# Optimization experiments

Hardware: AMD Instinct MI355X
Metric: run time of the kernel (lower is better)

Reference implementation:

```python
import math
import jax, jax.numpy as jnp
import numpy as np

B, T, C = 1, 2048, 2048
H, G, D = 16, 4, 128          # n_head, n_query_groups, head_size; C == H*D
Q_PER_KV = H // G
EPS = 1e-5


def _apply_rope_interleaved(x, cos, sin):
    # x: [B, T, h, D]; cos/sin: [T, D//2]; interleaved (GPT-J) style pairs
    x1 = x[..., 0::2]
    x2 = x[..., 1::2]
    c = cos[None, :, None, :]
    s = sin[None, :, None, :]
    o1 = x1 * c - x2 * s
    o2 = x1 * s + x2 * c
    return jnp.stack([o1, o2], axis=-1).reshape(x.shape)


def setup_inputs() -> dict:
    key = jax.random.key(0)
    k0, k1, k2, k3 = jax.random.split(key, 4)
    x = jax.random.normal(k0, (B, T, C), jnp.float32)
    # rotary cache (standard theta=10000)
    inv_freq = 1.0 / (10000.0 ** (np.arange(0, D, 2, dtype=np.float64) / D))
    ang = np.outer(np.arange(T, dtype=np.float64), inv_freq)
    cos = jnp.asarray(np.cos(ang), jnp.float32)
    sin = jnp.asarray(np.sin(ang), jnp.float32)
    # RetNet per-head decay mask: D[h,i,j] = gamma_h^(i-j) for i>=j else 0
    gammas = 1.0 - 2.0 ** (-5.0 - np.arange(H, dtype=np.float64))
    i = np.arange(T)[:, None]
    j = np.arange(T)[None, :]
    diff = np.maximum(i - j, 0).astype(np.float64)
    m = np.where(i >= j, gammas[:, None, None] ** diff[None], 0.0)
    mask = jnp.asarray(m, jnp.float32)
    std = 0.02
    W_reten = jax.random.normal(k1, (C, (H + 2 * G) * D), jnp.float32) * std
    W_gate = jax.random.normal(k2, (C, C), jnp.float32) * std
    W_proj = jax.random.normal(k3, (C, C), jnp.float32) * std
    return {"x": x, "cos": cos, "sin": sin, "mask": mask,
            "W_reten": W_reten, "W_gate": W_gate, "W_proj": W_proj,
            "max_seq_length": T}


def reference(x, cos, sin, mask, W_reten, W_gate, W_proj, max_seq_length):
    # fused qkv projection, grouped-query layout
    qkv = (x @ W_reten).reshape(B, T, G, Q_PER_KV + 2, D)
    q = qkv[..., :Q_PER_KV, :].reshape(B, T, H, D)
    k = qkv[..., Q_PER_KV:Q_PER_KV + 1, :].reshape(B, T, G, D)
    v = qkv[..., Q_PER_KV + 1:, :].reshape(B, T, G, D)
    q = _apply_rope_interleaved(q, cos, sin)
    k = _apply_rope_interleaved(k, cos, sin)
    # [B, h, T, D]
    q = q.transpose(0, 2, 1, 3)
    k = jnp.repeat(k.transpose(0, 2, 1, 3), Q_PER_KV, axis=1)
    v = jnp.repeat(v.transpose(0, 2, 1, 3), Q_PER_KV, axis=1)
    # parallel retention: masked (decay) scores, no softmax
    scale = 1.0 / math.sqrt(D)
    qk = jnp.einsum('bhtd,bhsd->bhts', q, k) * scale
    qk = qk * mask[None]
    y = jnp.einsum('bhts,bhsd->bhtd', qk, v)
    # group norm = RMSNorm (no weight) over head_size
    y = y.transpose(0, 2, 1, 3)  # [B, T, H, D]
    y = y * jax.lax.rsqrt(jnp.mean(y * y, axis=-1, keepdims=True) + EPS)
    y = y.reshape(B, T, C)
    g = jax.nn.silu(x @ W_gate)
    return (g * y) @ W_proj
```

## Files before the change

### kernel.cpp

```cpp
#include <hip/hip_runtime.h>
#include <hip/hip_bf16.h>
#include <cstdint>
#include <cstddef>

typedef __bf16 bf16x8 __attribute__((ext_vector_type(8)));
typedef __bf16 bf16x4 __attribute__((ext_vector_type(4)));
typedef __bf16 bf16x2 __attribute__((ext_vector_type(2)));
typedef float  f32x4  __attribute__((ext_vector_type(4)));
typedef float  f32x2  __attribute__((ext_vector_type(2)));

#define T_SEQ 2048
#define CDIM  2048
#define NH    16
#define NG    4
#define DH    128
#define NCHUNK 32

__device__ __forceinline__ void gl_lds16(const __bf16* g, __bf16* l) {
  __builtin_amdgcn_global_load_lds(
      (const __attribute__((address_space(1))) void*)g,
      (__attribute__((address_space(3))) void*)l, 16, 0, 0);
}

__global__ __launch_bounds__(256) void pre_kernel(
    const float* __restrict__ x, const float* __restrict__ Wr,
    const float* __restrict__ Wg, const float* __restrict__ Wp,
    __bf16* __restrict__ xb, __bf16* __restrict__ wtb, __bf16* __restrict__ wpb) {
  __shared__ __bf16 tile[64][68];
  int bid = blockIdx.x;
  int tid = threadIdx.x;
  if (bid < 2048) {
    size_t i = ((size_t)bid * 256 + tid) * 8;
    f32x4 a = *(const f32x4*)(x + i);
    f32x4 b = *(const f32x4*)(x + i + 4);
    bf16x8 o;
#pragma unroll
    for (int j = 0; j < 4; ++j) { o[j] = (__bf16)a[j]; o[4 + j] = (__bf16)b[j]; }
    *(bf16x8*)(xb + i) = o;
    return;
  }
  int rel = bid - 2048;
  const float* W; __bf16* Wt; int N;
  if (rel < 1536)      { W = Wr; Wt = wtb;                        N = 3072; }
  else if (rel < 2560) { W = Wg; Wt = wtb + (size_t)3072 * CDIM;  N = 2048; rel -= 1536; }
  else                 { W = Wp; Wt = wpb;                        N = 2048; rel -= 2560; }
  const int K = 2048;
  int k0 = (rel & 31) * 64, n0 = (rel >> 5) * 64;
  int c4 = (tid & 15) * 4, r = tid >> 4;
#pragma unroll
  for (int rr = 0; rr < 4; ++rr) {
    int row = r + rr * 16;
    f32x4 v = *(const f32x4*)(W + (size_t)(k0 + row) * N + n0 + c4);
#pragma unroll
    for (int j = 0; j < 4; ++j) tile[row][c4 + j] = (__bf16)v[j];
  }
  __syncthreads();
  int n = tid >> 2, seg = tid & 3;
  __bf16 vals[16];
#pragma unroll
  for (int j = 0; j < 16; ++j) vals[j] = tile[seg * 16 + j][n];
  __bf16* dst = Wt + (size_t)(n0 + n) * K + k0 + seg * 16;
  *(bf16x8*)(dst)     = *(bf16x8*)(&vals[0]);
  *(bf16x8*)(dst + 8) = *(bf16x8*)(&vals[8]);
}

__global__ __launch_bounds__(256) void ropevt_kernel(const float* __restrict__ qkv,
    const float* __restrict__ cosb, const float* __restrict__ sinb,
    __bf16* __restrict__ qb, __bf16* __restrict__ kb, __bf16* __restrict__ vtb) {
  __shared__ __bf16 vt[64][136];
  int bid = blockIdx.x;
  int tid = threadIdx.x;
  if (bid < 2048) {
    int t = bid;
    int w = tid >> 6, l = tid & 63;
    float c = cosb[t * 64 + l], s = sinb[t * 64 + l];
#pragma unroll
    for (int it = 0; it < 5; ++it) {
      int slot = w + it * 4;
      int g = slot / 5, j = slot % 5;
      const float* src = qkv + (size_t)t * 3072 + g * 768 + j * 128;
      f32x2 xv = *(const f32x2*)(src + 2 * l);
      bf16x2 o;
      o[0] = (__bf16)(xv[0] * c - xv[1] * s);
      o[1] = (__bf16)(xv[0] * s + xv[1] * c);
      __bf16* dst = (j < 4) ? (qb + ((size_t)(g * 4 + j) * T_SEQ + t) * DH)
                            : (kb + ((size_t)g * T_SEQ + t) * DH);
      *(bf16x2*)(dst + 2 * l) = o;
    }
    return;
  }
  int rel = bid - 2048;
  int g = rel >> 5, t0 = (rel & 31) * 64;
#pragma unroll
  for (int it = 0; it < 8; ++it) {
    int q = it * 256 + tid;
    int tt = q >> 5, dq = q & 31;
    f32x4 v = *(const f32x4*)(qkv + (size_t)(t0 + tt) * 3072 + g * 768 + 640 + dq * 4);
#pragma unroll
    for (int j = 0; j < 4; ++j) vt[tt][dq * 4 + j] = (__bf16)v[j];
  }
  __syncthreads();
  int d = tid >> 1, half = tid & 1;
  __bf16 outv[32];
#pragma unroll
  for (int j = 0; j < 32; ++j) outv[j] = vt[half * 32 + j][d];
  __bf16* dst = vtb + ((size_t)g * DH + d) * T_SEQ + t0 + half * 32;
#pragma unroll
  for (int q4 = 0; q4 < 4; ++q4) *(bf16x8*)(dst + q4 * 8) = *(bf16x8*)(&outv[q4 * 8]);
}

__global__ __launch_bounds__(256) void kt_kernel(const __bf16* __restrict__ kb,
                                                 __bf16* __restrict__ ktb) {
  __shared__ __bf16 tile[64][136];
  int g = blockIdx.x >> 5, t0 = (blockIdx.x & 31) * 64;
  int tid = threadIdx.x;
#pragma unroll
  for (int it = 0; it < 4; ++it) {
    int fg = it * 256 + tid;
    int tt = fg >> 4, gr = fg & 15;
    bf16x8 v = *(const bf16x8*)(kb + ((size_t)g * T_SEQ + t0 + tt) * DH + gr * 8);
    *(bf16x8*)(&tile[tt][gr * 8]) = v;
  }
  __syncthreads();
  int d = tid >> 1, half = tid & 1;
  __bf16 outv[32];
#pragma unroll
  for (int j = 0; j < 32; ++j) outv[j] = tile[half * 32 + j][d];
  __bf16* dst = ktb + ((size_t)g * DH + d) * T_SEQ + t0 + half * 32;
#pragma unroll
  for (int q4 = 0; q4 < 4; ++q4) *(bf16x8*)(dst + q4 * 8) = *(bf16x8*)(&outv[q4 * 8]);
}

__global__ __launch_bounds__(256) void u_kernel(const __bf16* __restrict__ vtb,
                                                const __bf16* __restrict__ ktb,
                                                float* __restrict__ Ut) {
  int h = blockIdx.x >> 5, c = blockIdx.x & 31, g = h >> 2;
  int tid = threadIdx.x;
  int w = tid >> 6, l = tid & 63, lr = l & 15, lg = l >> 4;
  float l2g = log2f(1.0f - exp2f(-5.0f - (float)h));
  float ginv = exp2f(-l2g);
  f32x4 acc[2][8] = {};
#pragma unroll
  for (int kk = 0; kk < 2; ++kk) {
    int j0 = kk * 32 + lg * 8;
    float w0 = exp2f(l2g * (float)(64 - j0));
    bf16x8 aw[2];
#pragma unroll
    for (int i = 0; i < 2; ++i) {
      bf16x8 av = *(const bf16x8*)(vtb + ((size_t)g * DH + w * 32 + i * 16 + lr) * T_SEQ
                                   + c * 64 + j0);
      float wj = w0;
#pragma unroll
      for (int jj = 0; jj < 8; ++jj) { aw[i][jj] = (__bf16)((float)av[jj] * wj); wj *= ginv; }
    }
#pragma unroll
    for (int jf = 0; jf < 8; ++jf) {
      bf16x8 bv = *(const bf16x8*)(ktb + ((size_t)g * DH + jf * 16 + lr) * T_SEQ
                                   + c * 64 + j0);
      acc[0][jf] = __builtin_amdgcn_mfma_f32_16x16x32_bf16(aw[0], bv, acc[0][jf], 0, 0, 0);
      acc[1][jf] = __builtin_amdgcn_mfma_f32_16x16x32_bf16(aw[1], bv, acc[1][jf], 0, 0, 0);
    }
  }
  float* outb = Ut + (size_t)blockIdx.x * 16384;
#pragma unroll
  for (int i = 0; i < 2; ++i)
#pragma unroll
    for (int jf = 0; jf < 8; ++jf)
#pragma unroll
      for (int r = 0; r < 4; ++r)
        outb[(w * 32 + i * 16 + lg * 4 + r) * 128 + jf * 16 + lr] = acc[i][jf][r];
}

__global__ __launch_bounds__(256) void scan_kernel(const float* __restrict__ Ut,
                                                   __bf16* __restrict__ St) {
  int bid = blockIdx.x, tid = threadIdx.x;
  int h = bid >> 4;
  int row = ((bid >> 1) & 7) * 16 + (tid >> 4);
  int col = (bid & 1) * 64 + (tid & 15) * 4;
  float l2g = log2f(1.0f - exp2f(-5.0f - (float)h));
  float df = exp2f(l2g * 64.0f);
  f32x4 s = {0.f, 0.f, 0.f, 0.f};
  for (int c = 0; c < NCHUNK; ++c) {
    size_t base = ((size_t)(h * NCHUNK + c) * 128 + row) * 128 + col;
    bf16x4 o;
#pragma unroll
    for (int j = 0; j < 4; ++j) o[j] = (__bf16)s[j];
    *(bf16x4*)(St + base) = o;
    f32x4 u = *(const f32x4*)(Ut + base);
#pragma unroll
    for (int j = 0; j < 4; ++j) s[j] = df * s[j] + u[j];
  }
}

__global__ __launch_bounds__(256) void attn2_kernel(const __bf16* __restrict__ qb,
    const __bf16* __restrict__ kb, const __bf16* __restrict__ vtb,
    const __bf16* __restrict__ St, float* __restrict__ y) {
  __shared__ __bf16 kl[64 * 128];
  __shared__ __bf16 vl[128 * 64];
  __shared__ __bf16 pl[4][16 * 64];
  int h = blockIdx.x >> 5, qt = blockIdx.x & 31;
  int g = h >> 2;
  int w = threadIdx.x >> 6, l = threadIdx.x & 63;
  int lr = l & 15, lg = l >> 4;
  int t0b = qt * 64;
  int t0 = t0b + w * 16;
  bf16x8 qf[4];
#pragma unroll
  for (int kbk = 0; kbk < 4; ++kbk)
    qf[kbk] = *(const bf16x8*)(qb + ((size_t)h * T_SEQ + t0 + lr) * DH + kbk * 32 + lg * 8);
  float gamma = 1.0f - exp2f(-5.0f - (float)h);
  float l2g = log2f(gamma);
  const float scale = 0.088388347648318447f;
  int s0 = t0b;
#pragma unroll
  for (int it = 0; it < 4; ++it) {
    int fg = it * 256 + threadIdx.x;
    {
      int ss = fg >> 4, gr = fg & 15;
      bf16x8 kv = *(const bf16x8*)(kb + ((size_t)g * T_SEQ + s0 + ss) * DH + gr * 8);
      *(bf16x8*)((char*)kl + ss * 256 + ((gr * 16) ^ ((ss & 7) << 4))) = kv;
    }
    {
      int d = fg >> 3, gv = fg & 7;
      bf16x8 vv = *(const bf16x8*)(vtb + ((size_t)g * DH + d) * T_SEQ + s0 + gv * 8);
      *(bf16x8*)((char*)vl + d * 128 + ((gv * 16) ^ ((d & 7) << 4))) = vv;
    }
  }
  float wfac = scale * exp2f(l2g * (float)(w * 16 + lr));
  bf16x8 qwf[4];
#pragma unroll
  for (int kbk = 0; kbk < 4; ++kbk)
#pragma unroll
    for (int e = 0; e < 8; ++e) qwf[kbk][e] = (__bf16)((float)qf[kbk][e] * wfac);
  f32x4 acc[8] = {};
  const __bf16* Sb = St + (size_t)(h * NCHUNK + qt) * 16384;
#pragma unroll
  for (int dc = 0; dc < 8; ++dc)
#pragma unroll
    for (int kc = 0; kc < 4; ++kc) {
      bf16x8 sf = *(const bf16x8*)(Sb + (dc * 16 + lr) * 128 + kc * 32 + lg * 8);
      acc[dc] = __builtin_amdgcn_mfma_f32_16x16x32_bf16(qwf[kc], sf, acc[dc], 0, 0, 0);
    }
  __syncthreads();
#pragma unroll
  for (int sc = 0; sc < 4; ++sc) {
    f32x4 p = {0.f, 0.f, 0.f, 0.f};
    int srow = sc * 16 + lr;
#pragma unroll
    for (int kbk = 0; kbk < 4; ++kbk) {
      bf16x8 kf = *(const bf16x8*)((char*)kl + srow * 256 +
                                   ((kbk * 64 + lg * 16) ^ ((srow & 7) << 4)));
      p = __builtin_amdgcn_mfma_f32_16x16x32_bf16(qf[kbk], kf, p, 0, 0, 0);
    }
#pragma unroll
    for (int r = 0; r < 4; ++r) {
      int tl = lg * 4 + r;
      int diff = (w * 16 + tl) - srow;
      float val = 0.0f;
      if (diff >= 0) val = p[r] * scale * exp2f((float)diff * l2g);
      *(__bf16*)((char*)(pl[w]) + tl * 128 +
                 (((sc * 16 + lr) * 2) ^ ((tl & 7) << 4))) = (__bf16)val;
    }
  }
  bf16x8 pa[2];
#pragma unroll
  for (int kc = 0; kc < 2; ++kc)
    pa[kc] = *(const bf16x8*)((char*)(pl[w]) + lr * 128 +
                              ((kc * 64 + lg * 16) ^ ((lr & 7) << 4)));
#pragma unroll
  for (int dc = 0; dc < 8; ++dc) {
#pragma unroll
    for (int kc = 0; kc < 2; ++kc) {
      int vrow = dc * 16 + lr;
      bf16x8 vf = *(const bf16x8*)((char*)vl + vrow * 128 +
                                   ((kc * 64 + lg * 16) ^ ((vrow & 7) << 4)));
      acc[dc] = __builtin_amdgcn_mfma_f32_16x16x32_bf16(pa[kc], vf, acc[dc], 0, 0, 0);
    }
  }
#pragma unroll
  for (int dc = 0; dc < 8; ++dc)
#pragma unroll
    for (int r = 0; r < 4; ++r)
      y[((size_t)h * T_SEQ + t0 + lg * 4 + r) * DH + dc * 16 + lr] = acc[dc][r];
}

template<int MODE>
__global__ __launch_bounds__(256) void gemm_gl_kernel(
    const __bf16* __restrict__ A, const __bf16* __restrict__ Bt,
    float* __restrict__ Cf, __bf16* __restrict__ Cg, int M, int N, int K) {
  __shared__ __bf16 Asb[64 * 64];
  __shared__ __bf16 Bsb[128 * 64];
  int m0 = blockIdx.x * 64, n0 = blockIdx.y * 128;
  int tid = threadIdx.x;
  int w = tid >> 6, l = tid & 63;
  int wr = w >> 1, wc = w & 1;
  int lr = l & 15, lg = l >> 4;
  int nk = K >> 6;
  const __bf16* Ab = A + (size_t)m0 * K;
  const __bf16* Bb = Bt + (size_t)n0 * K;
  f32x4 acc[2][4] = {};
  for (int kt = 0; kt < nk; ++kt) {
    int k0 = kt << 6;
#pragma unroll
    for (int c = 0; c < 2; ++c) {
      int ca = c * 256 + tid;
      int row = ca >> 3, kseg = ca & 7;
      gl_lds16(Ab + (size_t)row * K + k0 + ((kseg ^ (row & 7)) << 3), Asb + ca * 8);
    }
#pragma unroll
    for (int c = 0; c < 4; ++c) {
      int cb = c * 256 + tid;
      int row = cb >> 3, kseg = cb & 7;
      gl_lds16(Bb + (size_t)row * K + k0 + ((kseg ^ (row & 7)) << 3), Bsb + cb * 8);
    }
    __syncthreads();
    bf16x8 av[2][2], bv[4][2];
#pragma unroll
    for (int i = 0; i < 2; ++i)
#pragma unroll
      for (int kk = 0; kk < 2; ++kk) {
        int row = wr * 32 + i * 16 + lr;
        av[i][kk] = *(const bf16x8*)((const char*)Asb +
            ((row * 128 + kk * 64 + lg * 16) ^ ((lr & 7) << 4)));
      }
#pragma unroll
    for (int j = 0; j < 4; ++j)
#pragma unroll
      for (int kk = 0; kk < 2; ++kk) {
        int row = wc * 64 + j * 16 + lr;
        bv[j][kk] = *(const bf16x8*)((const char*)Bsb +
            ((row * 128 + kk * 64 + lg * 16) ^ ((lr & 7) << 4)));
      }
#pragma unroll
    for (int kk = 0; kk < 2; ++kk)
#pragma unroll
      for (int i = 0; i < 2; ++i)
#pragma unroll
        for (int j = 0; j < 4; ++j)
          acc[i][j] = __builtin_amdgcn_mfma_f32_16x16x32_bf16(av[i][kk], bv[j][kk],
                                                              acc[i][j], 0, 0, 0);
    __syncthreads();
  }
#pragma unroll
  for (int i = 0; i < 2; ++i) {
    int row = m0 + wr * 32 + i * 16 + lg * 4;
#pragma unroll
    for (int j = 0; j < 4; ++j) {
      int col = n0 + wc * 64 + j * 16 + lr;
#pragma unroll
      for (int r = 0; r < 4; ++r) {
        float z = acc[i][j][r];
        if (MODE == 0) {
          Cf[(size_t)(row + r) * N + col] = z;
        } else {
          if (n0 < 3072) {
            Cf[(size_t)(row + r) * 3072 + col] = z;
          } else {
            float sv = z / (1.0f + expf(-z));
            Cg[(size_t)(row + r) * 2048 + (col - 3072)] = (__bf16)sv;
          }
        }
      }
    }
  }
}

__global__ __launch_bounds__(256) void rms_gate_kernel(const float* __restrict__ y,
                                                       const __bf16* __restrict__ gateb,
                                                       __bf16* __restrict__ ynormb) {
  int f = blockIdx.x * 4 + (threadIdx.x >> 6);
  int l = threadIdx.x & 63;
  int h = f >> 11, t = f & 2047;
  const float* row = y + (size_t)f * DH;
  f32x2 v = *(const f32x2*)(row + 2 * l);
  float ss = v[0] * v[0] + v[1] * v[1];
#pragma unroll
  for (int o = 32; o > 0; o >>= 1) ss += __shfl_xor(ss, o, 64);
  float r = rsqrtf(ss * (1.0f / 128.0f) + 1e-5f);
  size_t base = (size_t)t * CDIM + h * DH + 2 * l;
  bf16x2 gv = *(const bf16x2*)(gateb + base);
  bf16x2 o;
  o[0] = (__bf16)(v[0] * r * (float)gv[0]);
  o[1] = (__bf16)(v[1] * r * (float)gv[1]);
  *(bf16x2*)(ynormb + base) = o;
}

extern "C" void kernel_launch(void* const* d_in, const int* in_sizes, int n_in,
                              void* d_out, int out_size, void* d_ws, size_t ws_size,
                              hipStream_t stream) {
  const float* x    = (const float*)d_in[0];
  const float* cosb = (const float*)d_in[1];
  const float* sinb = (const float*)d_in[2];
  const float* Wr   = (const float*)d_in[4];
  const float* Wg   = (const float*)d_in[5];
  const float* Wp   = (const float*)d_in[6];

  char* ws = (char*)d_ws;
  size_t off = 0;
  auto alloc = [&](size_t bytes) { void* p = ws + off; off += (bytes + 255) & ~(size_t)255; return p; };
  __bf16* xb     = (__bf16*)alloc((size_t)CDIM * CDIM * 2);
  __bf16* wtb    = (__bf16*)alloc((size_t)5120 * CDIM * 2);
  __bf16* wpb    = (__bf16*)alloc((size_t)CDIM * CDIM * 2);
  char*   qkvblk = (char*)  alloc((size_t)T_SEQ * 3072 * 4);
  __bf16* qb     = (__bf16*)alloc((size_t)NH * T_SEQ * DH * 2);
  __bf16* kbp    = (__bf16*)alloc((size_t)NG * T_SEQ * DH * 2);
  __bf16* vtb    = (__bf16*)alloc((size_t)NG * DH * T_SEQ * 2);
  __bf16* ktb    = (__bf16*)alloc((size_t)NG * DH * T_SEQ * 2);
  __bf16* gateb  = (__bf16*)alloc((size_t)CDIM * CDIM * 2);
  float*  Ut     = (float*) alloc((size_t)NH * NCHUNK * 128 * 128 * 4);
  __bf16* Stb    = (__bf16*)alloc((size_t)NH * NCHUNK * 128 * 128 * 2);
  float*  qkv    = (float*)qkvblk;
  float*  yb     = (float*)qkvblk;
  __bf16* ynormb = (__bf16*)(qkvblk + (size_t)16 * 1024 * 1024);

  pre_kernel<<<5632, 256, 0, stream>>>(x, Wr, Wg, Wp, xb, wtb, wpb);
  gemm_gl_kernel<1><<<dim3(32, 40), 256, 0, stream>>>(xb, wtb, qkv, gateb, 2048, 5120, 2048);
  ropevt_kernel<<<2048 + NG * 32, 256, 0, stream>>>(qkv, cosb, sinb, qb, kbp, vtb);
  kt_kernel<<<NG * 32, 256, 0, stream>>>(kbp, ktb);
  u_kernel<<<NH * NCHUNK, 256, 0, stream>>>(vtb, ktb, Ut);
  scan_kernel<<<NH * 16, 256, 0, stream>>>(Ut, Stb);
  attn2_kernel<<<NH * NCHUNK, 256, 0, stream>>>(qb, kbp, vtb, Stb, yb);
  rms_gate_kernel<<<NH * T_SEQ / 4, 256, 0, stream>>>(yb, gateb, ynormb);
  gemm_gl_kernel<0><<<dim3(32, 16), 256, 0, stream>>>(ynormb, wpb, (float*)d_out, nullptr,
                                                      2048, 2048, 2048);
}
```

Baseline: 181.6 us.

## Fuse K transpose into rope, merge chunk-state GEMM with scan, fold RMS-gate into attention

Three fusions. The K transpose (with rope) moves into the rope/V-transpose kernel. The per-chunk KV outer-product GEMM is merged with the decay scan so the fp32 Ut buffer is never written or read back. The RMSNorm and gate multiply move into the attention epilogue, which removes the fp32 y round trip and one launch. The trade-off is that the scan kernel now runs only 256 blocks, each doing a serial loop of small MFMAs over 32 chunks. The attention epilogue also issues scalar, strided gate loads and output stores.

New measurement: 172.0 us. 5.3% less time.

```diff
diff --git a/kernel.cpp b/kernel.cpp
--- a/kernel.cpp
+++ b/kernel.cpp
@@ -64,9 +64,10 @@
   *(bf16x8*)(dst + 8) = *(bf16x8*)(&vals[8]);
 }
 
-__global__ __launch_bounds__(256) void ropevt_kernel(const float* __restrict__ qkv,
+__global__ __launch_bounds__(256) void ropekt_kernel(const float* __restrict__ qkv,
     const float* __restrict__ cosb, const float* __restrict__ sinb,
-    __bf16* __restrict__ qb, __bf16* __restrict__ kb, __bf16* __restrict__ vtb) {
+    __bf16* __restrict__ qb, __bf16* __restrict__ kb,
+    __bf16* __restrict__ vtb, __bf16* __restrict__ ktb) {
   __shared__ __bf16 vt[64][136];
   int bid = blockIdx.x;
   int tid = threadIdx.x;
@@ -89,112 +90,94 @@
     }
     return;
   }
-  int rel = bid - 2048;
+  if (bid < 2176) {
+    int rel = bid - 2048;
+    int g = rel >> 5, t0 = (rel & 31) * 64;
+#pragma unroll
+    for (int it = 0; it < 8; ++it) {
+      int q = it * 256 + tid;
+      int tt = q >> 5, dq = q & 31;
+      f32x4 v = *(const f32x4*)(qkv + (size_t)(t0 + tt) * 3072 + g * 768 + 640 + dq * 4);
+#pragma unroll
+      for (int j = 0; j < 4; ++j) vt[tt][dq * 4 + j] = (__bf16)v[j];
+    }
+    __syncthreads();
+    int d = tid >> 1, half = tid & 1;
+    __bf16 outv[32];
+#pragma unroll
+    for (int j = 0; j < 32; ++j) outv[j] = vt[half * 32 + j][d];
+    __bf16* dst = vtb + ((size_t)g * DH + d) * T_SEQ + t0 + half * 32;
+#pragma unroll
+    for (int q4 = 0; q4 < 4; ++q4) *(bf16x8*)(dst + q4 * 8) = *(bf16x8*)(&outv[q4 * 8]);
+    return;
+  }
+  int rel = bid - 2176;
   int g = rel >> 5, t0 = (rel & 31) * 64;
 #pragma unroll
   for (int it = 0; it < 8; ++it) {
     int q = it * 256 + tid;
     int tt = q >> 5, dq = q & 31;
-    f32x4 v = *(const f32x4*)(qkv + (size_t)(t0 + tt) * 3072 + g * 768 + 640 + dq * 4);
-#pragma unroll
-    for (int j = 0; j < 4; ++j) vt[tt][dq * 4 + j] = (__bf16)v[j];
+    int t = t0 + tt;
+    f32x4 v = *(const f32x4*)(qkv + (size_t)t * 3072 + g * 768 + 512 + dq * 4);
+    float c0 = cosb[t * 64 + dq * 2],     s0 = sinb[t * 64 + dq * 2];
+    float c1 = cosb[t * 64 + dq * 2 + 1], s1 = sinb[t * 64 + dq * 2 + 1];
+    vt[tt][dq * 4 + 0] = (__bf16)(v[0] * c0 - v[1] * s0);
+    vt[tt][dq * 4 + 1] = (__bf16)(v[0] * s0 + v[1] * c0);
+    vt[tt][dq * 4 + 2] = (__bf16)(v[2] * c1 - v[3] * s1);
+    vt[tt][dq * 4 + 3] = (__bf16)(v[2] * s1 + v[3] * c1);
   }
   __syncthreads();
   int d = tid >> 1, half = tid & 1;
   __bf16 outv[32];
 #pragma unroll
   for (int j = 0; j < 32; ++j) outv[j] = vt[half * 32 + j][d];
-  __bf16* dst = vtb + ((size_t)g * DH + d) * T_SEQ + t0 + half * 32;
+  __bf16* dst = ktb + ((size_t)g * DH + d) * T_SEQ + t0 + half * 32;
 #pragma unroll
   for (int q4 = 0; q4 < 4; ++q4) *(bf16x8*)(dst + q4 * 8) = *(bf16x8*)(&outv[q4 * 8]);
 }
 
-__global__ __launch_bounds__(256) void kt_kernel(const __bf16* __restrict__ kb,
-                                                 __bf16* __restrict__ ktb) {
-  __shared__ __bf16 tile[64][136];
-  int g = blockIdx.x >> 5, t0 = (blockIdx.x & 31) * 64;
-  int tid = threadIdx.x;
-#pragma unroll
-  for (int it = 0; it < 4; ++it) {
-    int fg = it * 256 + tid;
-    int tt = fg >> 4, gr = fg & 15;
-    bf16x8 v = *(const bf16x8*)(kb + ((size_t)g * T_SEQ + t0 + tt) * DH + gr * 8);
-    *(bf16x8*)(&tile[tt][gr * 8]) = v;
-  }
-  __syncthreads();
-  int d = tid >> 1, half = tid & 1;
-  __bf16 outv[32];
-#pragma unroll
-  for (int j = 0; j < 32; ++j) outv[j] = tile[half * 32 + j][d];
-  __bf16* dst = ktb + ((size_t)g * DH + d) * T_SEQ + t0 + half * 32;
-#pragma unroll
-  for (int q4 = 0; q4 < 4; ++q4) *(bf16x8*)(dst + q4 * 8) = *(bf16x8*)(&outv[q4 * 8]);
-}
-
-__global__ __launch_bounds__(256) void u_kernel(const __bf16* __restrict__ vtb,
-                                                const __bf16* __restrict__ ktb,
-                                                float* __restrict__ Ut) {
-  int h = blockIdx.x >> 5, c = blockIdx.x & 31, g = h >> 2;
-  int tid = threadIdx.x;
-  int w = tid >> 6, l = tid & 63, lr = l & 15, lg = l >> 4;
+__global__ __launch_bounds__(256) void uscan_kernel(const __bf16* __restrict__ vtb,
+                                                    const __bf16* __restrict__ ktb,
+                                                    __bf16* __restrict__ St) {
+  int bid = blockIdx.x;
+  int h = bid >> 4, m = (bid >> 1) & 7, half = bid & 1;
+  int g = h >> 2;
+  int tid = threadIdx.x, w = tid >> 6, l = tid & 63, lr = l & 15, lg = l >> 4;
+  int jf = half * 4 + w;
   float l2g = log2f(1.0f - exp2f(-5.0f - (float)h));
   float ginv = exp2f(-l2g);
-  f32x4 acc[2][8] = {};
-#pragma unroll
-  for (int kk = 0; kk < 2; ++kk) {
-    int j0 = kk * 32 + lg * 8;
-    float w0 = exp2f(l2g * (float)(64 - j0));
-    bf16x8 aw[2];
-#pragma unroll
-    for (int i = 0; i < 2; ++i) {
-      bf16x8 av = *(const bf16x8*)(vtb + ((size_t)g * DH + w * 32 + i * 16 + lr) * T_SEQ
-                                   + c * 64 + j0);
-      float wj = w0;
-#pragma unroll
-      for (int jj = 0; jj < 8; ++jj) { aw[i][jj] = (__bf16)((float)av[jj] * wj); wj *= ginv; }
-    }
-#pragma unroll
-    for (int jf = 0; jf < 8; ++jf) {
-      bf16x8 bv = *(const bf16x8*)(ktb + ((size_t)g * DH + jf * 16 + lr) * T_SEQ
-                                   + c * 64 + j0);
-      acc[0][jf] = __builtin_amdgcn_mfma_f32_16x16x32_bf16(aw[0], bv, acc[0][jf], 0, 0, 0);
-      acc[1][jf] = __builtin_amdgcn_mfma_f32_16x16x32_bf16(aw[1], bv, acc[1][jf], 0, 0, 0);
-    }
-  }
-  float* outb = Ut + (size_t)blockIdx.x * 16384;
-#pragma unroll
-  for (int i = 0; i < 2; ++i)
-#pragma unroll
-    for (int jf = 0; jf < 8; ++jf)
-#pragma unroll
-      for (int r = 0; r < 4; ++r)
-        outb[(w * 32 + i * 16 + lg * 4 + r) * 128 + jf * 16 + lr] = acc[i][jf][r];
-}
-
-__global__ __launch_bounds__(256) void scan_kernel(const float* __restrict__ Ut,
-                                                   __bf16* __restrict__ St) {
-  int bid = blockIdx.x, tid = threadIdx.x;
-  int h = bid >> 4;
-  int row = ((bid >> 1) & 7) * 16 + (tid >> 4);
-  int col = (bid & 1) * 64 + (tid & 15) * 4;
-  float l2g = log2f(1.0f - exp2f(-5.0f - (float)h));
-  float df = exp2f(l2g * 64.0f);
-  f32x4 s = {0.f, 0.f, 0.f, 0.f};
+  float df   = exp2f(l2g * 64.0f);
+  float wk[2];
+#pragma unroll
+  for (int kk = 0; kk < 2; ++kk) wk[kk] = exp2f(l2g * (float)(64 - (kk * 32 + lg * 8)));
+  const __bf16* vrow = vtb + ((size_t)g * DH + m * 16 + lr) * T_SEQ;
+  const __bf16* krow = ktb + ((size_t)g * DH + jf * 16 + lr) * T_SEQ;
+  f32x4 S = {0.f, 0.f, 0.f, 0.f};
   for (int c = 0; c < NCHUNK; ++c) {
-    size_t base = ((size_t)(h * NCHUNK + c) * 128 + row) * 128 + col;
-    bf16x4 o;
-#pragma unroll
-    for (int j = 0; j < 4; ++j) o[j] = (__bf16)s[j];
-    *(bf16x4*)(St + base) = o;
-    f32x4 u = *(const f32x4*)(Ut + base);
-#pragma unroll
-    for (int j = 0; j < 4; ++j) s[j] = df * s[j] + u[j];
+    f32x4 u = {0.f, 0.f, 0.f, 0.f};
+#pragma unroll
+    for (int kk = 0; kk < 2; ++kk) {
+      int j0 = c * 64 + kk * 32 + lg * 8;
+      bf16x8 av = *(const bf16x8*)(vrow + j0);
+      bf16x8 bv = *(const bf16x8*)(krow + j0);
+      bf16x8 aw;
+      float wj = wk[kk];
+#pragma unroll
+      for (int jj = 0; jj < 8; ++jj) { aw[jj] = (__bf16)((float)av[jj] * wj); wj *= ginv; }
+      u = __builtin_amdgcn_mfma_f32_16x16x32_bf16(aw, bv, u, 0, 0, 0);
+    }
+    __bf16* out = St + ((size_t)(h * NCHUNK + c) * 128 + m * 16 + lg * 4) * 128 + jf * 16 + lr;
+#pragma unroll
+    for (int r = 0; r < 4; ++r) out[r * 128] = (__bf16)S[r];
+#pragma unroll
+    for (int r = 0; r < 4; ++r) S[r] = df * S[r] + u[r];
   }
 }
 
 __global__ __launch_bounds__(256) void attn2_kernel(const __bf16* __restrict__ qb,
     const __bf16* __restrict__ kb, const __bf16* __restrict__ vtb,
-    const __bf16* __restrict__ St, float* __restrict__ y) {
+    const __bf16* __restrict__ St, const __bf16* __restrict__ gateb,
+    __bf16* __restrict__ ynormb) {
   __shared__ __bf16 kl[64 * 128];
   __shared__ __bf16 vl[128 * 64];
   __shared__ __bf16 pl[4][16 * 64];
@@ -277,11 +260,26 @@
       acc[dc] = __builtin_amdgcn_mfma_f32_16x16x32_bf16(pa[kc], vf, acc[dc], 0, 0, 0);
     }
   }
+  float rs[4];
+#pragma unroll
+  for (int r = 0; r < 4; ++r) {
+    float ssum = 0.f;
+#pragma unroll
+    for (int dc = 0; dc < 8; ++dc) ssum += acc[dc][r] * acc[dc][r];
+    ssum += __shfl_xor(ssum, 1, 64);
+    ssum += __shfl_xor(ssum, 2, 64);
+    ssum += __shfl_xor(ssum, 4, 64);
+    ssum += __shfl_xor(ssum, 8, 64);
+    rs[r] = rsqrtf(ssum * (1.0f / 128.0f) + 1e-5f);
+  }
 #pragma unroll
   for (int dc = 0; dc < 8; ++dc)
 #pragma unroll
-    for (int r = 0; r < 4; ++r)
-      y[((size_t)h * T_SEQ + t0 + lg * 4 + r) * DH + dc * 16 + lr] = acc[dc][r];
+    for (int r = 0; r < 4; ++r) {
+      size_t idx = (size_t)(t0 + lg * 4 + r) * CDIM + h * DH + dc * 16 + lr;
+      float gv = (float)gateb[idx];
+      ynormb[idx] = (__bf16)(acc[dc][r] * rs[r] * gv);
+    }
 }
 
 template<int MODE>
@@ -365,26 +363,6 @@
   }
 }
 
-__global__ __launch_bounds__(256) void rms_gate_kernel(const float* __restrict__ y,
-                                                       const __bf16* __restrict__ gateb,
-                                                       __bf16* __restrict__ ynormb) {
-  int f = blockIdx.x * 4 + (threadIdx.x >> 6);
-  int l = threadIdx.x & 63;
-  int h = f >> 11, t = f & 2047;
-  const float* row = y + (size_t)f * DH;
-  f32x2 v = *(const f32x2*)(row + 2 * l);
-  float ss = v[0] * v[0] + v[1] * v[1];
-#pragma unroll
-  for (int o = 32; o > 0; o >>= 1) ss += __shfl_xor(ss, o, 64);
-  float r = rsqrtf(ss * (1.0f / 128.0f) + 1e-5f);
-  size_t base = (size_t)t * CDIM + h * DH + 2 * l;
-  bf16x2 gv = *(const bf16x2*)(gateb + base);
-  bf16x2 o;
-  o[0] = (__bf16)(v[0] * r * (float)gv[0]);
-  o[1] = (__bf16)(v[1] * r * (float)gv[1]);
-  *(bf16x2*)(ynormb + base) = o;
-}
-
 extern "C" void kernel_launch(void* const* d_in, const int* in_sizes, int n_in,
                               void* d_out, int out_size, void* d_ws, size_t ws_size,
                               hipStream_t stream) {
@@ -407,20 +385,15 @@
   __bf16* vtb    = (__bf16*)alloc((size_t)NG * DH * T_SEQ * 2);
   __bf16* ktb    = (__bf16*)alloc((size_t)NG * DH * T_SEQ * 2);
   __bf16* gateb  = (__bf16*)alloc((size_t)CDIM * CDIM * 2);
-  float*  Ut     = (float*) alloc((size_t)NH * NCHUNK * 128 * 128 * 4);
   __bf16* Stb    = (__bf16*)alloc((size_t)NH * NCHUNK * 128 * 128 * 2);
   float*  qkv    = (float*)qkvblk;
-  float*  yb     = (float*)qkvblk;
-  __bf16* ynormb = (__bf16*)(qkvblk + (size_t)16 * 1024 * 1024);
+  __bf16* ynormb = (__bf16*)qkvblk;
 
   pre_kernel<<<5632, 256, 0, stream>>>(x, Wr, Wg, Wp, xb, wtb, wpb);
   gemm_gl_kernel<1><<<dim3(32, 40), 256, 0, stream>>>(xb, wtb, qkv, gateb, 2048, 5120, 2048);
-  ropevt_kernel<<<2048 + NG * 32, 256, 0, stream>>>(qkv, cosb, sinb, qb, kbp, vtb);
-  kt_kernel<<<NG * 32, 256, 0, stream>>>(kbp, ktb);
-  u_kernel<<<NH * NCHUNK, 256, 0, stream>>>(vtb, ktb, Ut);
-  scan_kernel<<<NH * 16, 256, 0, stream>>>(Ut, Stb);
-  attn2_kernel<<<NH * NCHUNK, 256, 0, stream>>>(qb, kbp, vtb, Stb, yb);
-  rms_gate_kernel<<<NH * T_SEQ / 4, 256, 0, stream>>>(yb, gateb, ynormb);
+  ropekt_kernel<<<2048 + NG * 32 * 2, 256, 0, stream>>>(qkv, cosb, sinb, qb, kbp, vtb, ktb);
+  uscan_kernel<<<256, 256, 0, stream>>>(vtb, ktb, Stb);
+  attn2_kernel<<<NH * NCHUNK, 256, 0, stream>>>(qb, kbp, vtb, Stb, gateb, ynormb);
   gemm_gl_kernel<0><<<dim3(32, 16), 256, 0, stream>>>(ynormb, wpb, (float*)d_out, nullptr,
                                                       2048, 2048, 2048);
 }
```
